# Kernel optimization log

Hardware: AMD Instinct MI355X
Metric: run time of the kernel (lower is better)

The kernel has to match this reference:

```python
import jax, jax.numpy as jnp
import numpy as np

B, T, D = 256, 512, 128   # batch, T_max, input_dim
Z, TR, EM, RH = 128, 256, 256, 512  # z_dim, trans_dim, emission_dim, rnn_dim


def _dkf_infer(x, y, eps_comb, eps_emit, rnn_Wih, rnn_Whh, rnn_bih, rnn_bhh, h0, zq0,
               tr_g1_W, tr_g1_b, tr_g2_W, tr_g2_b, tr_p1_W, tr_p1_b, tr_p2_W, tr_p2_b,
               tr_mu_W, tr_mu_b, tr_lv_W, tr_lv_b,
               cb_h_W, cb_h_b, cb_mu_W, cb_mu_b, cb_lv_W, cb_lv_b,
               em_h1_W, em_h1_b, em_h2_W, em_h2_b, em_mu_W, em_mu_b, em_logvar):
    b = x.shape[0]
    # --- nn.RNN (relu nonlinearity, batch_first), scanned time-major ---
    xw = jnp.einsum('btd,dh->tbh', x, rnn_Wih) + rnn_bih  # [T,B,RH] input projection hoisted out of scan

    def rnn_step(h, xw_t):
        h = jax.nn.relu(xw_t + h @ rnn_Whh + rnn_bhh)
        return h, h

    _, rnn_out = jax.lax.scan(rnn_step, jnp.broadcast_to(h0, (b, h0.shape[0])), xw)  # [T,B,RH]

    y_tm = jnp.swapaxes(y, 0, 1)  # [T,B,D]

    def step(z_prev, inp):
        h_rnn, yt, e_cb, e_em = inp
        # GatedTransition (infer only uses prior mu/logvar; its sample is discarded)
        gate = jax.nn.sigmoid(jax.nn.relu(z_prev @ tr_g1_W + tr_g1_b) @ tr_g2_W + tr_g2_b)
        prop = jax.nn.relu(z_prev @ tr_p1_W + tr_p1_b) @ tr_p2_W + tr_p2_b
        pr_mu = (1.0 - gate) * (z_prev @ tr_mu_W + tr_mu_b) + gate * prop
        pr_lv = jax.nn.relu(prop) @ tr_lv_W + tr_lv_b
        # Combiner + reparameterization
        hc = 0.5 * (jnp.tanh(z_prev @ cb_h_W + cb_h_b) + h_rnn)
        mu = hc @ cb_mu_W + cb_mu_b
        lv = hc @ cb_lv_W + cb_lv_b
        z_t = mu + e_cb * jnp.exp(0.5 * lv)
        # Emitter + reparameterization
        h1 = jax.nn.relu(z_t @ em_h1_W + em_h1_b)
        h2 = jax.nn.relu(h1 @ em_h2_W + em_h2_b)
        x_mu = h2 @ em_mu_W + em_mu_b
        x_t = x_mu + e_em * jnp.exp(0.5 * em_logvar)
        # KL(q || prior) summed over z, per batch element
        kl = jnp.sum(0.5 * (pr_lv - lv + (jnp.exp(lv) + (mu - pr_mu) ** 2) / jnp.exp(pr_lv) - 1.0), axis=1)
        # per-element MSE reduced over x_dim
        rec = jnp.mean((x_t - yt) ** 2, axis=1)
        return z_t, (kl, rec)

    z0 = jnp.broadcast_to(zq0, (b, zq0.shape[0]))
    _, (kl_states, rec_losses) = jax.lax.scan(step, z0, (rnn_out, y_tm, eps_comb, eps_emit))
    return jnp.stack([jnp.mean(rec_losses), jnp.mean(kl_states)])  # [rec_loss, kl_loss]


def setup_inputs() -> dict:
    key = jax.random.key(0)
    ks = iter(jax.random.split(key, 32))
    nrm = lambda shape, s=0.05: jax.random.normal(next(ks), shape, dtype=jnp.float32) * s
    z = lambda *shape: jnp.zeros(shape, jnp.float32)
    return dict(
        x=nrm((B, T, D), 1.0), y=nrm((B, T, D), 1.0),
        eps_comb=nrm((T, B, Z), 1.0), eps_emit=nrm((T, B, D), 1.0),
        rnn_Wih=nrm((D, RH)), rnn_Whh=nrm((RH, RH)), rnn_bih=z(RH), rnn_bhh=z(RH),
        h0=z(RH), zq0=z(Z),
        tr_g1_W=nrm((Z, TR)), tr_g1_b=z(TR), tr_g2_W=nrm((TR, Z)), tr_g2_b=z(Z),
        tr_p1_W=nrm((Z, TR)), tr_p1_b=z(TR), tr_p2_W=nrm((TR, Z)), tr_p2_b=z(Z),
        tr_mu_W=jnp.eye(Z, dtype=jnp.float32), tr_mu_b=z(Z),  # identity init as in torch code
        tr_lv_W=nrm((Z, Z)), tr_lv_b=z(Z),
        cb_h_W=nrm((Z, RH)), cb_h_b=z(RH),
        cb_mu_W=nrm((RH, Z)), cb_mu_b=z(Z),
        cb_lv_W=nrm((RH, Z)), cb_lv_b=z(Z),
        em_h1_W=nrm((Z, EM)), em_h1_b=z(EM),
        em_h2_W=nrm((EM, EM)), em_h2_b=z(EM),
        em_mu_W=nrm((EM, D)), em_mu_b=z(D),
        em_logvar=jnp.ones((D,), jnp.float32),  # nn.Parameter(torch.ones(input_dim))
    )


def reference(x, y, eps_comb, eps_emit, rnn_Wih, rnn_Whh, rnn_bih, rnn_bhh, h0, zq0,
              tr_g1_W, tr_g1_b, tr_g2_W, tr_g2_b, tr_p1_W, tr_p1_b, tr_p2_W, tr_p2_b,
              tr_mu_W, tr_mu_b, tr_lv_W, tr_lv_b,
              cb_h_W, cb_h_b, cb_mu_W, cb_mu_b, cb_lv_W, cb_lv_b,
              em_h1_W, em_h1_b, em_h2_W, em_h2_b, em_mu_W, em_mu_b, em_logvar):
    return _dkf_infer(x, y, eps_comb, eps_emit, rnn_Wih, rnn_Whh, rnn_bih, rnn_bhh, h0, zq0,
                      tr_g1_W, tr_g1_b, tr_g2_W, tr_g2_b, tr_p1_W, tr_p1_b, tr_p2_W, tr_p2_b,
                      tr_mu_W, tr_mu_b, tr_lv_W, tr_lv_b,
                      cb_h_W, cb_h_b, cb_mu_W, cb_mu_b, cb_lv_W, cb_lv_b,
                      em_h1_W, em_h1_b, em_h2_W, em_h2_b, em_mu_W, em_mu_b, em_logvar)
```

## Files before the change

kernel.cpp:

```cpp
#include <hip/hip_runtime.h>


#define T_LEN 512
#define BATCH 256
#define DIMX  128
#define ZDIM  128
#define RHD   512
#define CHUNK 32

typedef _Float16 f16;
typedef _Float16 f16x4 __attribute__((ext_vector_type(4)));
typedef _Float16 f16x8 __attribute__((ext_vector_type(8)));
typedef float    f32x4 __attribute__((ext_vector_type(4)));

#define MFMA16(a,b,c) __builtin_amdgcn_mfma_f32_16x16x32_f16((a),(b),(c),0,0,0)

#define PK_WIH  0u
#define PK_WHH  65536u
#define PK_G1   327680u
#define PK_G2   360448u
#define PK_P1   393216u
#define PK_P2   425984u
#define PK_TMU  458752u
#define PK_TLV  475136u
#define PK_CBH  491520u
#define PK_CBML 557056u
#define PK_E1   688128u
#define PK_E2   720896u
#define PK_EMU  786432u

#define WS_XW   0ull
#define WS_Z    (WS_XW  + 134217728ull)
#define WS_MU   (WS_Z   + 33619968ull)
#define WS_LV   (WS_MU  + 33554432ull)
#define WS_PK   (WS_LV  + 33554432ull)
#define WS_PART (WS_PK  + 1638400ull)
#define WS_PROG (WS_PART + 16384ull)
#define WS_END  (WS_PROG + 256ull)

__device__ __forceinline__ void ldsfence() {
  asm volatile("s_waitcnt lgkmcnt(0)" ::: "memory");
  __builtin_amdgcn_sched_barrier(0);
}

__device__ __forceinline__ void lbar() {
  asm volatile("s_waitcnt lgkmcnt(0)" ::: "memory");
  __builtin_amdgcn_s_barrier();
  asm volatile("" ::: "memory");
}

__device__ __forceinline__ void pin8(f16x8& v) {
  f32x4 t = __builtin_bit_cast(f32x4, v);
  asm volatile("" : "+v"(t));
  v = __builtin_bit_cast(f16x8, t);
}

template<int N>
__device__ __forceinline__ void zacc(f32x4* a) {
  f32x4 z = {0.f, 0.f, 0.f, 0.f};
#pragma unroll
  for (int i = 0; i < N; ++i) a[i] = z;
}

__device__ __forceinline__ f16x8 cvt8(const float* p) {
  float4 a = *(const float4*)p, b = *(const float4*)(p + 4);
  f16x8 r;
  r[0] = (f16)a.x; r[1] = (f16)a.y; r[2] = (f16)a.z; r[3] = (f16)a.w;
  r[4] = (f16)b.x; r[5] = (f16)b.y; r[6] = (f16)b.z; r[7] = (f16)b.w;
  return r;
}

__device__ __forceinline__ int swz(int row, int col) {
  return (row << 9) + (col ^ ((row & 7) << 3));
}
__device__ __forceinline__ int swz128(int row, int col) {
  return (row << 7) + (col ^ ((row & 7) << 3));
}

template<int KS>
__device__ __forceinline__ void load_af(const f16* src, int sstr, int lane, f16x8* af) {
#pragma unroll
  for (int ks = 0; ks < KS; ++ks)
    af[ks] = *(const f16x8*)(src + (lane & 15) * sstr + ks * 32 + ((lane >> 4) << 3));
}

template<int KS, int NT>
__device__ __forceinline__ void gemm_regA(const f16x8* af, const f16* __restrict__ bp,
                                          int lane, f32x4* acc) {
#pragma unroll
  for (int ks = 0; ks < KS; ++ks)
#pragma unroll
    for (int j = 0; j < NT; ++j) {
      f16x8 bf = *(const f16x8*)(bp + (((size_t)(ks * NT + j)) << 9) + (lane << 3));
      acc[j] = MFMA16(af[ks], bf, acc[j]);
    }
}

template<int NT>
__device__ __forceinline__ void store_relu(const f32x4* acc, const float* __restrict__ bias,
                                           f16* dst, int dstr, int lane) {
  int colv = lane & 15, rb = (lane >> 4) << 2;
#pragma unroll
  for (int j = 0; j < NT; ++j)
#pragma unroll
    for (int r = 0; r < 4; ++r)
      dst[(rb + r) * dstr + j * 16 + colv] = (f16)fmaxf(acc[j][r] + bias[j * 16 + colv], 0.f);
}

struct PackEnt { const float* s1; const float* s2; int nsplit, K, N; unsigned dst, wg0; };
struct PackTab { PackEnt e[13]; };

__global__ void pack_all_kernel(PackTab tb, f16* __restrict__ pk) {
  int i = 0;
#pragma unroll
  for (int k = 1; k < 13; ++k)
    if (blockIdx.x >= tb.e[k].wg0) i = k;
  const PackEnt& E = tb.e[i];
  int idx = (blockIdx.x - E.wg0) * 256 + threadIdx.x;
  if (idx >= E.K * E.N) return;
  int j = idx & 7, l = (idx >> 3) & 63, fi = idx >> 9;
  int NTt = E.N >> 4;
  int nt = fi % NTt, ks = fi / NTt;
  int k = ks * 32 + ((l >> 4) << 3) + j;
  int n = (nt << 4) + (l & 15);
  float v;
  if (n < E.nsplit) v = E.s1[(size_t)k * E.nsplit + n];
  else              v = E.s2[(size_t)k * (E.N - E.nsplit) + (n - E.nsplit)];
  pk[E.dst + idx] = (f16)v;
}

__global__ void zero_prog_kernel(unsigned* __restrict__ p) {
  if (threadIdx.x < 16)
    __hip_atomic_store(p + threadIdx.x, 0u, __ATOMIC_RELAXED, __HIP_MEMORY_SCOPE_AGENT);
}

__global__ __launch_bounds__(256) void xw_kernel(
    const float* __restrict__ x, const f16* __restrict__ pk,
    const float* __restrict__ bih, const float* __restrict__ bhh,
    f16* __restrict__ xw) {
  __shared__ float bs[512];
  const int tid = threadIdx.x, lane = tid & 63, w = tid >> 6;
  const int colv = lane & 15, l4 = lane >> 4;
  const int m0 = blockIdx.x * 64 + w * 16;
  const int t = m0 >> 8, b0 = m0 & 255;
  for (int i = tid; i < 512; i += 256) bs[i] = bih[i] + bhh[i];
  __syncthreads();
  f16x8 xB[4];
  const float* xr = x + ((size_t)(b0 + colv) * T_LEN + t) * DIMX;
#pragma unroll
  for (int ks = 0; ks < 4; ++ks) xB[ks] = cvt8(xr + ks * 32 + l4 * 8);
  f32x4 acc[32]; zacc<32>(acc);
#pragma unroll
  for (int ks = 0; ks < 4; ++ks)
#pragma unroll
    for (int mt = 0; mt < 32; ++mt)
      acc[mt] = MFMA16(*(const f16x8*)(pk + PK_WIH + ((size_t)(ks * 32 + mt) << 9) + (lane << 3)),
                       xB[ks], acc[mt]);
  f16* xo = xw + ((size_t)t * BATCH + b0 + colv) * RHD;
#pragma unroll
  for (int mt = 0; mt < 32; ++mt) {
    f16x4 v;
#pragma unroll
    for (int r = 0; r < 4; ++r) v[r] = (f16)(acc[mt][r] + bs[mt * 16 + l4 * 4 + r]);
    *(f16x4*)(xo + mt * 16 + l4 * 4) = v;
  }
}

__global__ __launch_bounds__(256, 1) void scan_pipe_kernel(
    const f16* __restrict__ pk, const float* __restrict__ h0,
    const float* __restrict__ zq0, const float* __restrict__ chb,
    const float* __restrict__ cmb, const float* __restrict__ clb,
    const float* __restrict__ eps_comb, f16* __restrict__ xw,
    f16* __restrict__ z_all, f16* __restrict__ mu_all, f16* __restrict__ lv_all,
    unsigned* __restrict__ prog) {
  __shared__ __align__(16) f16 lds[73728];
  const int tid = threadIdx.x, lane = tid & 63, w = tid >> 6;
  const int colv = lane & 15, l4 = lane >> 4;

  if (blockIdx.x < 16) {
    const int g = blockIdx.x, b0 = g * 16;
    f16* whh_lds = lds;
    f16* h_st = lds + 65536;
    {
      const uint4* src = (const uint4*)(pk + PK_WHH + 196608u);
      for (int i = tid; i < 8192; i += 256) ((uint4*)whh_lds)[i] = src[i];
    }
    f16x8 whhA[8][12];
#pragma unroll
    for (int mt = 0; mt < 8; ++mt)
#pragma unroll
      for (int ks = 0; ks < 12; ++ks) {
        whhA[mt][ks] = *(const f16x8*)(pk + PK_WHH +
            ((size_t)(ks * 32 + w * 8 + mt) << 9) + (lane << 3));
        pin8(whhA[mt][ks]);
      }
    for (int i = tid; i < 8192; i += 256) h_st[swz(i >> 9, i & 511)] = (f16)h0[i & 511];
    __syncthreads();

    const int moff = w * 128 + l4 * 4;
    f16* xp = xw + (size_t)(b0 + colv) * RHD;
    f16x4 xwc[8], xwn[8];
#pragma unroll
    for (int mt = 0; mt < 8; ++mt) xwc[mt] = *(const f16x4*)(xp + moff + mt * 16);

    for (int c = 0; c < T_LEN / CHUNK; ++c) {
#pragma unroll 1
      for (int tt = 0; tt < CHUNK; ++tt) {
        int t = c * CHUNK + tt;
        f16* xpn = (t < T_LEN - 1) ? xp + (size_t)BATCH * RHD : xp;
#pragma unroll
        for (int mt = 0; mt < 8; ++mt) xwn[mt] = *(const f16x4*)(xpn + moff + mt * 16);
        f32x4 acc[8]; zacc<8>(acc);
#pragma unroll
        for (int ks = 0; ks < 12; ++ks) {
          f16x8 B = *(const f16x8*)&h_st[swz(colv, ks * 32 + l4 * 8)];
#pragma unroll
          for (int mt = 0; mt < 8; ++mt) acc[mt] = MFMA16(whhA[mt][ks], B, acc[mt]);
        }
#pragma unroll
        for (int ks = 0; ks < 4; ++ks) {
          f16x8 B = *(const f16x8*)&h_st[swz(colv, (12 + ks) * 32 + l4 * 8)];
#pragma unroll
          for (int mt = 0; mt < 8; ++mt)
            acc[mt] = MFMA16(*(const f16x8*)(whh_lds +
                (((ks * 32 + w * 8 + mt) << 6) + lane) * 8), B, acc[mt]);
        }
        lbar();
#pragma unroll
        for (int mt = 0; mt < 8; ++mt) {
          f16x4 h4;
#pragma unroll
          for (int r = 0; r < 4; ++r)
            h4[r] = (f16)fmaxf(acc[mt][r] + (float)xwc[mt][r], 0.f);
          *(f16x4*)&h_st[swz(colv, moff + mt * 16)] = h4;
          *(f16x4*)(xp + moff + mt * 16) = h4;
        }
        lbar();
        xp = xpn;
#pragma unroll
        for (int mt = 0; mt < 8; ++mt) xwc[mt] = xwn[mt];
      }
      __syncthreads();
      if (tid == 0)
        __hip_atomic_store(prog + g, (unsigned)(c + 1), __ATOMIC_RELEASE,
                           __HIP_MEMORY_SCOPE_AGENT);
    }
  } else {
    const int g = blockIdx.x - 16, b0 = g * 16;
    f16* cbml_lds = lds;
    f16* hc_st = lds + 32768;
    f16* z_st  = lds + 40960;
    f16* m_st  = lds + 43008;
    {
      const uint4* src = (const uint4*)(pk + PK_CBML + 98304u);
      for (int i = tid; i < 4096; i += 256) ((uint4*)cbml_lds)[i] = src[i];
    }
    f16x8 cbhA[8][4];
#pragma unroll
    for (int mt = 0; mt < 8; ++mt)
#pragma unroll
      for (int ks = 0; ks < 4; ++ks) {
        cbhA[mt][ks] = *(const f16x8*)(pk + PK_CBH +
            ((size_t)(ks * 32 + w * 8 + mt) << 9) + (lane << 3));
        pin8(cbhA[mt][ks]);
      }
    f16x8 cbmlA[4][12];
#pragma unroll
    for (int mt = 0; mt < 4; ++mt)
#pragma unroll
      for (int ks = 0; ks < 12; ++ks) {
        cbmlA[mt][ks] = *(const f16x8*)(pk + PK_CBML +
            ((size_t)(ks * 16 + w * 4 + mt) << 9) + (lane << 3));
        pin8(cbmlA[mt][ks]);
      }
    f16x4 chbv[8];
#pragma unroll
    for (int mt = 0; mt < 8; ++mt)
#pragma unroll
      for (int r = 0; r < 4; ++r)
        chbv[mt][r] = (f16)chb[(w * 8 + mt) * 16 + l4 * 4 + r];
    float mb[4][4];
#pragma unroll
    for (int mt = 0; mt < 4; ++mt)
#pragma unroll
      for (int r = 0; r < 4; ++r) {
        int d = (w * 4 + mt) * 16 + l4 * 4 + r;
        mb[mt][r] = (d < 128) ? cmb[d] : clb[d - 128];
      }
    for (int i = tid; i < 2048; i += 256) {
      f16 zv = (f16)zq0[i & 127];
      z_st[swz128(i >> 7, i & 127)] = zv;
      z_all[(size_t)(b0 + (i >> 7)) * ZDIM + (i & 127)] = zv;
    }
    __syncthreads();

    const int moff = w * 128 + l4 * 4;
    const int m2off = w * 64 + l4 * 4;
    const int be = tid >> 4, d0 = (tid & 15) * 8;
    const f16* hp = xw + (size_t)(b0 + colv) * RHD;
    const float* epb = eps_comb + (size_t)(b0 + be) * ZDIM + d0;
    f16x4 hv[8];
    float4 ep0, ep1, epn0, epn1;

    for (int c = 0; c < T_LEN / CHUNK; ++c) {
      if (tid == 0) {
        while (__hip_atomic_load(prog + g, __ATOMIC_RELAXED,
                                 __HIP_MEMORY_SCOPE_AGENT) < (unsigned)(c + 1))
          __builtin_amdgcn_s_sleep(2);
      }
      __syncthreads();
      __builtin_amdgcn_fence(__ATOMIC_ACQUIRE, "agent");
      {
        const f16* hpt = hp + (size_t)(c * CHUNK) * BATCH * RHD;
#pragma unroll
        for (int mt = 0; mt < 8; ++mt) hv[mt] = *(const f16x4*)(hpt + moff + mt * 16);
        const float* ept = epb + (size_t)(c * CHUNK) * BATCH * ZDIM;
        ep0 = *(const float4*)ept; ep1 = *(const float4*)(ept + 4);
      }
#pragma unroll 1
      for (int tt = 0; tt < CHUNK; ++tt) {
        int t = c * CHUNK + tt;
        f16x8 zB[4];
#pragma unroll
        for (int ks = 0; ks < 4; ++ks)
          zB[ks] = *(const f16x8*)&z_st[swz128(colv, ks * 32 + l4 * 8)];
        f32x4 a1[8]; zacc<8>(a1);
#pragma unroll
        for (int ks = 0; ks < 4; ++ks)
#pragma unroll
          for (int mt = 0; mt < 8; ++mt) a1[mt] = MFMA16(cbhA[mt][ks], zB[ks], a1[mt]);
#pragma unroll
        for (int mt = 0; mt < 8; ++mt) {
          f16x4 hc4;
#pragma unroll
          for (int r = 0; r < 4; ++r) {
            float cs = a1[mt][r] + (float)chbv[mt][r];
            float ex = __builtin_amdgcn_exp2f(cs * 2.885390082f);
            float th = 1.f - 2.f * __builtin_amdgcn_rcpf(ex + 1.f);
            hc4[r] = (f16)(0.5f * (th + (float)hv[mt][r]));
          }
          *(f16x4*)&hc_st[swz(colv, moff + mt * 16)] = hc4;
        }
        lbar();
        if (tt < CHUNK - 1) {
          const f16* hpt = hp + (size_t)(t + 1) * BATCH * RHD;
#pragma unroll
          for (int mt = 0; mt < 8; ++mt) hv[mt] = *(const f16x4*)(hpt + moff + mt * 16);
          const float* ept = epb + (size_t)(t + 1) * BATCH * ZDIM;
          epn0 = *(const float4*)ept; epn1 = *(const float4*)(ept + 4);
        }
        f32x4 a2[4]; zacc<4>(a2);
#pragma unroll
        for (int ks = 0; ks < 12; ++ks) {
          f16x8 hcB = *(const f16x8*)&hc_st[swz(colv, ks * 32 + l4 * 8)];
#pragma unroll
          for (int mt = 0; mt < 4; ++mt) a2[mt] = MFMA16(cbmlA[mt][ks], hcB, a2[mt]);
        }
#pragma unroll
        for (int ks = 0; ks < 4; ++ks) {
          f16x8 hcB = *(const f16x8*)&hc_st[swz(colv, (12 + ks) * 32 + l4 * 8)];
#pragma unroll
          for (int mt = 0; mt < 4; ++mt)
            a2[mt] = MFMA16(*(const f16x8*)(cbml_lds +
                (((ks * 16 + w * 4 + mt) << 6) + lane) * 8), hcB, a2[mt]);
        }
#pragma unroll
        for (int mt = 0; mt < 4; ++mt) {
          f16x4 v;
#pragma unroll
          for (int r = 0; r < 4; ++r) v[r] = (f16)(a2[mt][r] + mb[mt][r]);
          *(f16x4*)&m_st[colv * 264 + m2off + mt * 16] = v;
        }
        lbar();
        {
          f16x8 mu8 = *(const f16x8*)&m_st[be * 264 + d0];
          f16x8 lv8 = *(const f16x8*)&m_st[be * 264 + 128 + d0];
          float epv[8] = {ep0.x, ep0.y, ep0.z, ep0.w, ep1.x, ep1.y, ep1.z, ep1.w};
          f16x8 z8;
#pragma unroll
          for (int r = 0; r < 8; ++r) {
            float mu = (float)mu8[r], lv = (float)lv8[r];
            z8[r] = (f16)(mu + epv[r] * __builtin_amdgcn_exp2f(lv * 0.7213475204f));
          }
          *(f16x8*)&z_st[swz128(be, d0)] = z8;
          size_t o = ((size_t)t * BATCH + b0 + be) * ZDIM + d0;
          *(f16x8*)(z_all + o + (size_t)BATCH * ZDIM) = z8;
          *(f16x8*)(mu_all + o) = mu8;
          *(f16x8*)(lv_all + o) = lv8;
        }
        lbar();
        ep0 = epn0; ep1 = epn1;
      }
    }
  }
}

__global__ __launch_bounds__(256) void dpar_kernel(
    const f16* __restrict__ z_all, const f16* __restrict__ mu_all,
    const f16* __restrict__ lv_all, const float* __restrict__ y,
    const float* __restrict__ eps_emit, const f16* __restrict__ pk,
    const float* __restrict__ g1b, const float* __restrict__ g2b,
    const float* __restrict__ p1b, const float* __restrict__ p2b,
    const float* __restrict__ tmub, const float* __restrict__ tlvb,
    const float* __restrict__ e1b, const float* __restrict__ e2b,
    const float* __restrict__ emub, const float* __restrict__ em_logvar,
    float* __restrict__ partials) {
  __shared__ __align__(16) f16 sb256[4][16 * 264];
  __shared__ __align__(16) f16 sb128[4][16 * 136];
  __shared__ float wsum[4][2];
  const int tid = threadIdx.x, lane = tid & 63, w = tid >> 6;
  const int colv = lane & 15, rb = (lane >> 4) << 2;
  const int m0 = blockIdx.x * 64 + w * 16;
  const int t = m0 >> 8, b0 = m0 & 255;
  f16* B256 = &sb256[w][0];
  f16* B128 = &sb128[w][0];

  f16x8 zp[4], zt[4];
  const f16* zpr = z_all + ((size_t)t * BATCH + b0) * ZDIM;
#pragma unroll
  for (int ks = 0; ks < 4; ++ks) {
    zp[ks] = *(const f16x8*)(zpr + (size_t)colv * ZDIM + ks * 32 + ((lane >> 4) << 3));
    zt[ks] = *(const f16x8*)(zpr + (size_t)BATCH * ZDIM + (size_t)colv * ZDIM + ks * 32 + ((lane >> 4) << 3));
  }

  f32x4 a16[16], a8[8];
  f16x8 af[8], af4[4];
  zacc<16>(a16); gemm_regA<4, 16>(zp, pk + PK_G1, lane, a16);
  store_relu<16>(a16, g1b, B256, 264, lane); ldsfence();
  load_af<8>(B256, 264, lane, af); ldsfence();
  zacc<8>(a8); gemm_regA<8, 8>(af, pk + PK_G2, lane, a8);
  f32x4 gate[8];
#pragma unroll
  for (int j = 0; j < 8; ++j)
#pragma unroll
    for (int r = 0; r < 4; ++r)
      gate[j][r] = 1.f / (1.f + expf(-(a8[j][r] + g2b[j * 16 + colv])));
  zacc<16>(a16); gemm_regA<4, 16>(zp, pk + PK_P1, lane, a16);
  store_relu<16>(a16, p1b, B256, 264, lane); ldsfence();
  load_af<8>(B256, 264, lane, af); ldsfence();
  zacc<8>(a8); gemm_regA<8, 8>(af, pk + PK_P2, lane, a8);
  f32x4 prop[8];
#pragma unroll
  for (int j = 0; j < 8; ++j)
#pragma unroll
    for (int r = 0; r < 4; ++r) {
      float v = a8[j][r] + p2b[j * 16 + colv];
      prop[j][r] = v;
      B128[(rb + r) * 136 + j * 16 + colv] = (f16)fmaxf(v, 0.f);
    }
  ldsfence();
  zacc<8>(a8); gemm_regA<4, 8>(zp, pk + PK_TMU, lane, a8);
  f32x4 prmu[8];
#pragma unroll
  for (int j = 0; j < 8; ++j)
#pragma unroll
    for (int r = 0; r < 4; ++r) {
      float gg = gate[j][r];
      prmu[j][r] = (1.f - gg) * (a8[j][r] + tmub[j * 16 + colv]) + gg * prop[j][r];
    }
  load_af<4>(B128, 136, lane, af4); ldsfence();
  zacc<8>(a8); gemm_regA<4, 8>(af4, pk + PK_TLV, lane, a8);
  f32x4 prlv[8];
#pragma unroll
  for (int j = 0; j < 8; ++j)
#pragma unroll
    for (int r = 0; r < 4; ++r) prlv[j][r] = a8[j][r] + tlvb[j * 16 + colv];
  zacc<16>(a16); gemm_regA<4, 16>(zt, pk + PK_E1, lane, a16);
  store_relu<16>(a16, e1b, B256, 264, lane); ldsfence();
  load_af<8>(B256, 264, lane, af); ldsfence();
  zacc<16>(a16); gemm_regA<8, 16>(af, pk + PK_E2, lane, a16);
  store_relu<16>(a16, e2b, B256, 264, lane); ldsfence();
  load_af<8>(B256, 264, lane, af); ldsfence();
  zacc<8>(a8); gemm_regA<8, 8>(af, pk + PK_EMU, lane, a8);
  float srec = 0.f, skl = 0.f;
#pragma unroll
  for (int j = 0; j < 8; ++j)
#pragma unroll
    for (int r = 0; r < 4; ++r) {
      int row = rb + r, n = j * 16 + colv;
      size_t tb = (size_t)t * BATCH + b0 + row;
      float xt = a8[j][r] + emub[n] + eps_emit[tb * DIMX + n] * expf(0.5f * em_logvar[n]);
      float dy = xt - y[((size_t)(b0 + row) * T_LEN + t) * DIMX + n];
      srec += dy * dy;
      float m_ = (float)mu_all[tb * ZDIM + n], l_ = (float)lv_all[tb * ZDIM + n];
      float dm = m_ - prmu[j][r];
      skl += 0.5f * (prlv[j][r] - l_ + (expf(l_) + dm * dm) * expf(-prlv[j][r]) - 1.f);
    }
#pragma unroll
  for (int off = 32; off; off >>= 1) {
    srec += __shfl_xor(srec, off);
    skl += __shfl_xor(skl, off);
  }
  if (lane == 0) { wsum[w][0] = srec; wsum[w][1] = skl; }
  __syncthreads();
  if (tid == 0) {
    partials[blockIdx.x * 2 + 0] = wsum[0][0] + wsum[1][0] + wsum[2][0] + wsum[3][0];
    partials[blockIdx.x * 2 + 1] = wsum[0][1] + wsum[1][1] + wsum[2][1] + wsum[3][1];
  }
}

__global__ void finalize_kernel(const float* __restrict__ partials, float* __restrict__ out) {
  __shared__ float sm[256][2];
  int tid = threadIdx.x;
  float r = 0.f, kk = 0.f;
  for (int i = tid; i < 2048; i += 256) {
    r += partials[2 * i];
    kk += partials[2 * i + 1];
  }
  sm[tid][0] = r; sm[tid][1] = kk;
  __syncthreads();
  for (int off = 128; off; off >>= 1) {
    if (tid < off) { sm[tid][0] += sm[tid + off][0]; sm[tid][1] += sm[tid + off][1]; }
    __syncthreads();
  }
  if (tid == 0) {
    out[0] = sm[0][0] / (131072.f * 128.f);
    out[1] = sm[0][1] / 131072.f;
  }
}

extern "C" void kernel_launch(void* const* d_in, const int* in_sizes, int n_in,
                              void* d_out, int out_size, void* d_ws, size_t ws_size,
                              hipStream_t stream) {
  (void)in_sizes; (void)n_in; (void)out_size;
  const float* x        = (const float*)d_in[0];
  const float* y        = (const float*)d_in[1];
  const float* eps_comb = (const float*)d_in[2];
  const float* eps_emit = (const float*)d_in[3];
  const float* wih = (const float*)d_in[4];
  const float* whh = (const float*)d_in[5];
  const float* bih = (const float*)d_in[6];
  const float* bhh = (const float*)d_in[7];
  const float* h0  = (const float*)d_in[8];
  const float* zq0 = (const float*)d_in[9];
  const float* g1W = (const float*)d_in[10]; const float* g1b = (const float*)d_in[11];
  const float* g2W = (const float*)d_in[12]; const float* g2b = (const float*)d_in[13];
  const float* p1W = (const float*)d_in[14]; const float* p1b = (const float*)d_in[15];
  const float* p2W = (const float*)d_in[16]; const float* p2b = (const float*)d_in[17];
  const float* tmuW = (const float*)d_in[18]; const float* tmub = (const float*)d_in[19];
  const float* tlvW = (const float*)d_in[20]; const float* tlvb = (const float*)d_in[21];
  const float* chW = (const float*)d_in[22]; const float* chb = (const float*)d_in[23];
  const float* cmW = (const float*)d_in[24]; const float* cmb = (const float*)d_in[25];
  const float* clW = (const float*)d_in[26]; const float* clb = (const float*)d_in[27];
  const float* e1W = (const float*)d_in[28]; const float* e1b = (const float*)d_in[29];
  const float* e2W = (const float*)d_in[30]; const float* e2b = (const float*)d_in[31];
  const float* emW = (const float*)d_in[32]; const float* emb = (const float*)d_in[33];
  const float* elv = (const float*)d_in[34];

  char* ws = (char*)d_ws;
  f16*  xw      = (f16*)(ws + WS_XW);
  f16*  z_all   = (f16*)(ws + WS_Z);
  f16*  mu_all  = (f16*)(ws + WS_MU);
  f16*  lv_all  = (f16*)(ws + WS_LV);
  f16*  pk      = (f16*)(ws + WS_PK);
  float* partials = (float*)(ws + WS_PART);
  unsigned* prog  = (unsigned*)(ws + WS_PROG);
  float* out = (float*)d_out;
  if (ws_size < WS_END) return;

  zero_prog_kernel<<<dim3(1), dim3(32), 0, stream>>>(prog);

  PackTab tb;
  unsigned wg = 0; int ei = 0;
#define PACK(S1, S2, NS_, K_, N_, OFF) \
  tb.e[ei] = PackEnt{S1, S2, NS_, K_, N_, OFF, wg}; wg += (unsigned)((K_) * (N_)) / 256; ++ei;
  PACK(wih, wih, 512, 128, 512, PK_WIH);
  PACK(whh, whh, 512, 512, 512, PK_WHH);
  PACK(g1W, g1W, 256, 128, 256, PK_G1);
  PACK(g2W, g2W, 128, 256, 128, PK_G2);
  PACK(p1W, p1W, 256, 128, 256, PK_P1);
  PACK(p2W, p2W, 128, 256, 128, PK_P2);
  PACK(tmuW, tmuW, 128, 128, 128, PK_TMU);
  PACK(tlvW, tlvW, 128, 128, 128, PK_TLV);
  PACK(chW, chW, 512, 128, 512, PK_CBH);
  PACK(cmW, clW, 128, 512, 256, PK_CBML);
  PACK(e1W, e1W, 256, 128, 256, PK_E1);
  PACK(e2W, e2W, 256, 256, 256, PK_E2);
  PACK(emW, emW, 128, 256, 128, PK_EMU);
#undef PACK
  pack_all_kernel<<<dim3(wg), dim3(256), 0, stream>>>(tb, pk);

  xw_kernel<<<dim3(2048), dim3(256), 0, stream>>>(x, pk, bih, bhh, xw);
  scan_pipe_kernel<<<dim3(32), dim3(256), 0, stream>>>(
      pk, h0, zq0, chb, cmb, clb, eps_comb, xw, z_all, mu_all, lv_all, prog);
  dpar_kernel<<<dim3(2048), dim3(256), 0, stream>>>(z_all, mu_all, lv_all, y, eps_emit, pk,
                                                    g1b, g2b, p1b, p2b, tmub, tlvb, e1b, e2b,
                                                    emb, elv, partials);
  finalize_kernel<<<dim3(1), dim3(256), 0, stream>>>(partials, out);
}
```

Measured before the change: 2.523 ms.

## Fuse input projection, recurrent scan and loss kernel into one persistent pipelined kernel

```diff
diff --git a/kernel.cpp b/kernel.cpp
--- a/kernel.cpp
+++ b/kernel.cpp
@@ -7,6 +7,7 @@
 #define ZDIM  128
 #define RHD   512
 #define CHUNK 32
+#define NWKR  224
 
 typedef _Float16 f16;
 typedef _Float16 f16x4 __attribute__((ext_vector_type(4)));
@@ -105,6 +106,10 @@
 #pragma unroll
     for (int r = 0; r < 4; ++r)
       dst[(rb + r) * dstr + j * 16 + colv] = (f16)fmaxf(acc[j][r] + bias[j * 16 + colv], 0.f);
+}
+
+__device__ __forceinline__ unsigned ldflag(const unsigned* p) {
+  return __hip_atomic_load(p, __ATOMIC_RELAXED, __HIP_MEMORY_SCOPE_AGENT);
 }
 
 struct PackEnt { const float* s1; const float* s2; int nsplit, K, N; unsigned dst, wg0; };
@@ -130,52 +135,31 @@
 }
 
 __global__ void zero_prog_kernel(unsigned* __restrict__ p) {
-  if (threadIdx.x < 16)
+  if (threadIdx.x < 48)
     __hip_atomic_store(p + threadIdx.x, 0u, __ATOMIC_RELAXED, __HIP_MEMORY_SCOPE_AGENT);
 }
 
-__global__ __launch_bounds__(256) void xw_kernel(
-    const float* __restrict__ x, const f16* __restrict__ pk,
-    const float* __restrict__ bih, const float* __restrict__ bhh,
-    f16* __restrict__ xw) {
-  __shared__ float bs[512];
-  const int tid = threadIdx.x, lane = tid & 63, w = tid >> 6;
-  const int colv = lane & 15, l4 = lane >> 4;
-  const int m0 = blockIdx.x * 64 + w * 16;
-  const int t = m0 >> 8, b0 = m0 & 255;
-  for (int i = tid; i < 512; i += 256) bs[i] = bih[i] + bhh[i];
-  __syncthreads();
-  f16x8 xB[4];
-  const float* xr = x + ((size_t)(b0 + colv) * T_LEN + t) * DIMX;
-#pragma unroll
-  for (int ks = 0; ks < 4; ++ks) xB[ks] = cvt8(xr + ks * 32 + l4 * 8);
-  f32x4 acc[32]; zacc<32>(acc);
-#pragma unroll
-  for (int ks = 0; ks < 4; ++ks)
-#pragma unroll
-    for (int mt = 0; mt < 32; ++mt)
-      acc[mt] = MFMA16(*(const f16x8*)(pk + PK_WIH + ((size_t)(ks * 32 + mt) << 9) + (lane << 3)),
-                       xB[ks], acc[mt]);
-  f16* xo = xw + ((size_t)t * BATCH + b0 + colv) * RHD;
-#pragma unroll
-  for (int mt = 0; mt < 32; ++mt) {
-    f16x4 v;
-#pragma unroll
-    for (int r = 0; r < 4; ++r) v[r] = (f16)(acc[mt][r] + bs[mt * 16 + l4 * 4 + r]);
-    *(f16x4*)(xo + mt * 16 + l4 * 4) = v;
-  }
-}
-
-__global__ __launch_bounds__(256, 1) void scan_pipe_kernel(
+__global__ __launch_bounds__(256, 1) void fused_kernel(
     const f16* __restrict__ pk, const float* __restrict__ h0,
     const float* __restrict__ zq0, const float* __restrict__ chb,
     const float* __restrict__ cmb, const float* __restrict__ clb,
     const float* __restrict__ eps_comb, f16* __restrict__ xw,
     f16* __restrict__ z_all, f16* __restrict__ mu_all, f16* __restrict__ lv_all,
-    unsigned* __restrict__ prog) {
+    const float* __restrict__ x, const float* __restrict__ bih,
+    const float* __restrict__ bhh, const float* __restrict__ y,
+    const float* __restrict__ eps_emit,
+    const float* __restrict__ g1b, const float* __restrict__ g2b,
+    const float* __restrict__ p1b, const float* __restrict__ p2b,
+    const float* __restrict__ tmub, const float* __restrict__ tlvb,
+    const float* __restrict__ e1b, const float* __restrict__ e2b,
+    const float* __restrict__ emub, const float* __restrict__ em_logvar,
+    float* __restrict__ partials, unsigned* __restrict__ flags) {
   __shared__ __align__(16) f16 lds[73728];
   const int tid = threadIdx.x, lane = tid & 63, w = tid >> 6;
   const int colv = lane & 15, l4 = lane >> 4;
+  unsigned* prog  = flags;
+  unsigned* zprog = flags + 16;
+  unsigned* xcnt  = flags + 32;
 
   if (blockIdx.x < 16) {
     const int g = blockIdx.x, b0 = g * 16;
@@ -197,6 +181,10 @@
     for (int i = tid; i < 8192; i += 256) h_st[swz(i >> 9, i & 511)] = (f16)h0[i & 511];
     __syncthreads();
 
+    if (tid == 0) { while (ldflag(xcnt + 0) < 128u) __builtin_amdgcn_s_sleep(2); }
+    __syncthreads();
+    __builtin_amdgcn_fence(__ATOMIC_ACQUIRE, "agent");
+
     const int moff = w * 128 + l4 * 4;
     f16* xp = xw + (size_t)(b0 + colv) * RHD;
     f16x4 xwc[8], xwn[8];
@@ -204,6 +192,10 @@
     for (int mt = 0; mt < 8; ++mt) xwc[mt] = *(const f16x4*)(xp + moff + mt * 16);
 
     for (int c = 0; c < T_LEN / CHUNK; ++c) {
+      const int cw = (c + 1 < 16) ? c + 1 : 15;
+      if (tid == 0) { while (ldflag(xcnt + cw) < 128u) __builtin_amdgcn_s_sleep(2); }
+      __syncthreads();
+      __builtin_amdgcn_fence(__ATOMIC_ACQUIRE, "agent");
 #pragma unroll 1
       for (int tt = 0; tt < CHUNK; ++tt) {
         int t = c * CHUNK + tt;
@@ -245,7 +237,7 @@
         __hip_atomic_store(prog + g, (unsigned)(c + 1), __ATOMIC_RELEASE,
                            __HIP_MEMORY_SCOPE_AGENT);
     }
-  } else {
+  } else if (blockIdx.x < 32) {
     const int g = blockIdx.x - 16, b0 = g * 16;
     f16* cbml_lds = lds;
     f16* hc_st = lds + 32768;
@@ -304,9 +296,7 @@
 
     for (int c = 0; c < T_LEN / CHUNK; ++c) {
       if (tid == 0) {
-        while (__hip_atomic_load(prog + g, __ATOMIC_RELAXED,
-                                 __HIP_MEMORY_SCOPE_AGENT) < (unsigned)(c + 1))
-          __builtin_amdgcn_s_sleep(2);
+        while (ldflag(prog + g) < (unsigned)(c + 1)) __builtin_amdgcn_s_sleep(2);
       }
       __syncthreads();
       __builtin_amdgcn_fence(__ATOMIC_ACQUIRE, "agent");
@@ -391,111 +381,149 @@
         lbar();
         ep0 = epn0; ep1 = epn1;
       }
-    }
-  }
-}
-
-__global__ __launch_bounds__(256) void dpar_kernel(
-    const f16* __restrict__ z_all, const f16* __restrict__ mu_all,
-    const f16* __restrict__ lv_all, const float* __restrict__ y,
-    const float* __restrict__ eps_emit, const f16* __restrict__ pk,
-    const float* __restrict__ g1b, const float* __restrict__ g2b,
-    const float* __restrict__ p1b, const float* __restrict__ p2b,
-    const float* __restrict__ tmub, const float* __restrict__ tlvb,
-    const float* __restrict__ e1b, const float* __restrict__ e2b,
-    const float* __restrict__ emub, const float* __restrict__ em_logvar,
-    float* __restrict__ partials) {
-  __shared__ __align__(16) f16 sb256[4][16 * 264];
-  __shared__ __align__(16) f16 sb128[4][16 * 136];
-  __shared__ float wsum[4][2];
-  const int tid = threadIdx.x, lane = tid & 63, w = tid >> 6;
-  const int colv = lane & 15, rb = (lane >> 4) << 2;
-  const int m0 = blockIdx.x * 64 + w * 16;
-  const int t = m0 >> 8, b0 = m0 & 255;
-  f16* B256 = &sb256[w][0];
-  f16* B128 = &sb128[w][0];
-
-  f16x8 zp[4], zt[4];
-  const f16* zpr = z_all + ((size_t)t * BATCH + b0) * ZDIM;
-#pragma unroll
-  for (int ks = 0; ks < 4; ++ks) {
-    zp[ks] = *(const f16x8*)(zpr + (size_t)colv * ZDIM + ks * 32 + ((lane >> 4) << 3));
-    zt[ks] = *(const f16x8*)(zpr + (size_t)BATCH * ZDIM + (size_t)colv * ZDIM + ks * 32 + ((lane >> 4) << 3));
-  }
-
-  f32x4 a16[16], a8[8];
-  f16x8 af[8], af4[4];
-  zacc<16>(a16); gemm_regA<4, 16>(zp, pk + PK_G1, lane, a16);
-  store_relu<16>(a16, g1b, B256, 264, lane); ldsfence();
-  load_af<8>(B256, 264, lane, af); ldsfence();
-  zacc<8>(a8); gemm_regA<8, 8>(af, pk + PK_G2, lane, a8);
-  f32x4 gate[8];
-#pragma unroll
-  for (int j = 0; j < 8; ++j)
-#pragma unroll
-    for (int r = 0; r < 4; ++r)
-      gate[j][r] = 1.f / (1.f + expf(-(a8[j][r] + g2b[j * 16 + colv])));
-  zacc<16>(a16); gemm_regA<4, 16>(zp, pk + PK_P1, lane, a16);
-  store_relu<16>(a16, p1b, B256, 264, lane); ldsfence();
-  load_af<8>(B256, 264, lane, af); ldsfence();
-  zacc<8>(a8); gemm_regA<8, 8>(af, pk + PK_P2, lane, a8);
-  f32x4 prop[8];
-#pragma unroll
-  for (int j = 0; j < 8; ++j)
-#pragma unroll
-    for (int r = 0; r < 4; ++r) {
-      float v = a8[j][r] + p2b[j * 16 + colv];
-      prop[j][r] = v;
-      B128[(rb + r) * 136 + j * 16 + colv] = (f16)fmaxf(v, 0.f);
-    }
-  ldsfence();
-  zacc<8>(a8); gemm_regA<4, 8>(zp, pk + PK_TMU, lane, a8);
-  f32x4 prmu[8];
-#pragma unroll
-  for (int j = 0; j < 8; ++j)
-#pragma unroll
-    for (int r = 0; r < 4; ++r) {
-      float gg = gate[j][r];
-      prmu[j][r] = (1.f - gg) * (a8[j][r] + tmub[j * 16 + colv]) + gg * prop[j][r];
-    }
-  load_af<4>(B128, 136, lane, af4); ldsfence();
-  zacc<8>(a8); gemm_regA<4, 8>(af4, pk + PK_TLV, lane, a8);
-  f32x4 prlv[8];
-#pragma unroll
-  for (int j = 0; j < 8; ++j)
-#pragma unroll
-    for (int r = 0; r < 4; ++r) prlv[j][r] = a8[j][r] + tlvb[j * 16 + colv];
-  zacc<16>(a16); gemm_regA<4, 16>(zt, pk + PK_E1, lane, a16);
-  store_relu<16>(a16, e1b, B256, 264, lane); ldsfence();
-  load_af<8>(B256, 264, lane, af); ldsfence();
-  zacc<16>(a16); gemm_regA<8, 16>(af, pk + PK_E2, lane, a16);
-  store_relu<16>(a16, e2b, B256, 264, lane); ldsfence();
-  load_af<8>(B256, 264, lane, af); ldsfence();
-  zacc<8>(a8); gemm_regA<8, 8>(af, pk + PK_EMU, lane, a8);
-  float srec = 0.f, skl = 0.f;
-#pragma unroll
-  for (int j = 0; j < 8; ++j)
-#pragma unroll
-    for (int r = 0; r < 4; ++r) {
-      int row = rb + r, n = j * 16 + colv;
-      size_t tb = (size_t)t * BATCH + b0 + row;
-      float xt = a8[j][r] + emub[n] + eps_emit[tb * DIMX + n] * expf(0.5f * em_logvar[n]);
-      float dy = xt - y[((size_t)(b0 + row) * T_LEN + t) * DIMX + n];
-      srec += dy * dy;
-      float m_ = (float)mu_all[tb * ZDIM + n], l_ = (float)lv_all[tb * ZDIM + n];
-      float dm = m_ - prmu[j][r];
-      skl += 0.5f * (prlv[j][r] - l_ + (expf(l_) + dm * dm) * expf(-prlv[j][r]) - 1.f);
-    }
-#pragma unroll
-  for (int off = 32; off; off >>= 1) {
-    srec += __shfl_xor(srec, off);
-    skl += __shfl_xor(skl, off);
-  }
-  if (lane == 0) { wsum[w][0] = srec; wsum[w][1] = skl; }
-  __syncthreads();
-  if (tid == 0) {
-    partials[blockIdx.x * 2 + 0] = wsum[0][0] + wsum[1][0] + wsum[2][0] + wsum[3][0];
-    partials[blockIdx.x * 2 + 1] = wsum[0][1] + wsum[1][1] + wsum[2][1] + wsum[3][1];
+      __syncthreads();
+      if (tid == 0)
+        __hip_atomic_store(zprog + g, (unsigned)(c + 1), __ATOMIC_RELEASE,
+                           __HIP_MEMORY_SCOPE_AGENT);
+    }
+  } else {
+    const int wkr = blockIdx.x - 32;
+    float* bs = (float*)lds;
+    for (int i = tid; i < 512; i += 256) bs[i] = bih[i] + bhh[i];
+    __syncthreads();
+    for (int i = wkr; i < 2048; i += NWKR) {
+      const int m0 = i * 64 + w * 16;
+      const int t = m0 >> 8, b0 = m0 & 255;
+      f16x8 xB[4];
+      const float* xr = x + ((size_t)(b0 + colv) * T_LEN + t) * DIMX;
+#pragma unroll
+      for (int ks = 0; ks < 4; ++ks) xB[ks] = cvt8(xr + ks * 32 + l4 * 8);
+      f32x4 acc[32]; zacc<32>(acc);
+#pragma unroll
+      for (int ks = 0; ks < 4; ++ks)
+#pragma unroll
+        for (int mt = 0; mt < 32; ++mt)
+          acc[mt] = MFMA16(*(const f16x8*)(pk + PK_WIH +
+              ((size_t)(ks * 32 + mt) << 9) + (lane << 3)), xB[ks], acc[mt]);
+      f16* xo = xw + ((size_t)t * BATCH + b0 + colv) * RHD;
+#pragma unroll
+      for (int mt = 0; mt < 32; ++mt) {
+        f16x4 v;
+#pragma unroll
+        for (int r = 0; r < 4; ++r) v[r] = (f16)(acc[mt][r] + bs[mt * 16 + l4 * 4 + r]);
+        *(f16x4*)(xo + mt * 16 + l4 * 4) = v;
+      }
+      __syncthreads();
+      if (tid == 0)
+        __hip_atomic_fetch_add(xcnt + (i >> 7), 1u, __ATOMIC_RELEASE,
+                               __HIP_MEMORY_SCOPE_AGENT);
+    }
+    for (int j = wkr; j < 2048; j += NWKR) {
+      const int m0 = j * 64 + w * 16;
+      const int t = m0 >> 8, b0 = m0 & 255;
+      const int c = j >> 7;
+      const int gb = (j & 3) * 4;
+      if (tid == 0) {
+        const unsigned need = (unsigned)(c + 1);
+        for (;;) {
+          unsigned a = ldflag(zprog + gb), b = ldflag(zprog + gb + 1);
+          unsigned cc = ldflag(zprog + gb + 2), d = ldflag(zprog + gb + 3);
+          unsigned mn = min(min(a, b), min(cc, d));
+          if (mn >= need) break;
+          __builtin_amdgcn_s_sleep(32);
+        }
+      }
+      __syncthreads();
+      __builtin_amdgcn_fence(__ATOMIC_ACQUIRE, "agent");
+
+      f16* B256 = lds + w * 4224;
+      f16* B128 = lds + 16896 + w * 2176;
+      float* wsum = (float*)(lds + 25600);
+      const int rb = (lane >> 4) << 2;
+
+      f16x8 zp[4], zt[4];
+      const f16* zpr = z_all + ((size_t)t * BATCH + b0) * ZDIM;
+#pragma unroll
+      for (int ks = 0; ks < 4; ++ks) {
+        zp[ks] = *(const f16x8*)(zpr + (size_t)colv * ZDIM + ks * 32 + (l4 << 3));
+        zt[ks] = *(const f16x8*)(zpr + (size_t)BATCH * ZDIM + (size_t)colv * ZDIM + ks * 32 + (l4 << 3));
+      }
+      f32x4 a16[16], a8[8];
+      f16x8 af[8], af4[4];
+      zacc<16>(a16); gemm_regA<4, 16>(zp, pk + PK_G1, lane, a16);
+      store_relu<16>(a16, g1b, B256, 264, lane); ldsfence();
+      load_af<8>(B256, 264, lane, af); ldsfence();
+      zacc<8>(a8); gemm_regA<8, 8>(af, pk + PK_G2, lane, a8);
+      f32x4 gate[8];
+#pragma unroll
+      for (int jj = 0; jj < 8; ++jj)
+#pragma unroll
+        for (int r = 0; r < 4; ++r)
+          gate[jj][r] = 1.f / (1.f + expf(-(a8[jj][r] + g2b[jj * 16 + colv])));
+      zacc<16>(a16); gemm_regA<4, 16>(zp, pk + PK_P1, lane, a16);
+      store_relu<16>(a16, p1b, B256, 264, lane); ldsfence();
+      load_af<8>(B256, 264, lane, af); ldsfence();
+      zacc<8>(a8); gemm_regA<8, 8>(af, pk + PK_P2, lane, a8);
+      f32x4 prop[8];
+#pragma unroll
+      for (int jj = 0; jj < 8; ++jj)
+#pragma unroll
+        for (int r = 0; r < 4; ++r) {
+          float v = a8[jj][r] + p2b[jj * 16 + colv];
+          prop[jj][r] = v;
+          B128[(rb + r) * 136 + jj * 16 + colv] = (f16)fmaxf(v, 0.f);
+        }
+      ldsfence();
+      zacc<8>(a8); gemm_regA<4, 8>(zp, pk + PK_TMU, lane, a8);
+      f32x4 prmu[8];
+#pragma unroll
+      for (int jj = 0; jj < 8; ++jj)
+#pragma unroll
+        for (int r = 0; r < 4; ++r) {
+          float gg = gate[jj][r];
+          prmu[jj][r] = (1.f - gg) * (a8[jj][r] + tmub[jj * 16 + colv]) + gg * prop[jj][r];
+        }
+      load_af<4>(B128, 136, lane, af4); ldsfence();
+      zacc<8>(a8); gemm_regA<4, 8>(af4, pk + PK_TLV, lane, a8);
+      f32x4 prlv[8];
+#pragma unroll
+      for (int jj = 0; jj < 8; ++jj)
+#pragma unroll
+        for (int r = 0; r < 4; ++r) prlv[jj][r] = a8[jj][r] + tlvb[jj * 16 + colv];
+      zacc<16>(a16); gemm_regA<4, 16>(zt, pk + PK_E1, lane, a16);
+      store_relu<16>(a16, e1b, B256, 264, lane); ldsfence();
+      load_af<8>(B256, 264, lane, af); ldsfence();
+      zacc<16>(a16); gemm_regA<8, 16>(af, pk + PK_E2, lane, a16);
+      store_relu<16>(a16, e2b, B256, 264, lane); ldsfence();
+      load_af<8>(B256, 264, lane, af); ldsfence();
+      zacc<8>(a8); gemm_regA<8, 8>(af, pk + PK_EMU, lane, a8);
+      float srec = 0.f, skl = 0.f;
+#pragma unroll
+      for (int jj = 0; jj < 8; ++jj)
+#pragma unroll
+        for (int r = 0; r < 4; ++r) {
+          int row = rb + r, n = jj * 16 + colv;
+          size_t tb = (size_t)t * BATCH + b0 + row;
+          float xt = a8[jj][r] + emub[n] + eps_emit[tb * DIMX + n] * expf(0.5f * em_logvar[n]);
+          float dy = xt - y[((size_t)(b0 + row) * T_LEN + t) * DIMX + n];
+          srec += dy * dy;
+          float m_ = (float)mu_all[tb * ZDIM + n], l_ = (float)lv_all[tb * ZDIM + n];
+          float dm = m_ - prmu[jj][r];
+          skl += 0.5f * (prlv[jj][r] - l_ + (expf(l_) + dm * dm) * expf(-prlv[jj][r]) - 1.f);
+        }
+#pragma unroll
+      for (int off = 32; off; off >>= 1) {
+        srec += __shfl_xor(srec, off);
+        skl += __shfl_xor(skl, off);
+      }
+      if (lane == 0) { wsum[w * 2] = srec; wsum[w * 2 + 1] = skl; }
+      __syncthreads();
+      if (tid == 0) {
+        partials[j * 2 + 0] = wsum[0] + wsum[2] + wsum[4] + wsum[6];
+        partials[j * 2 + 1] = wsum[1] + wsum[3] + wsum[5] + wsum[7];
+      }
+      __syncthreads();
+    }
   }
 }
 
@@ -554,11 +582,11 @@
   f16*  lv_all  = (f16*)(ws + WS_LV);
   f16*  pk      = (f16*)(ws + WS_PK);
   float* partials = (float*)(ws + WS_PART);
-  unsigned* prog  = (unsigned*)(ws + WS_PROG);
+  unsigned* flags = (unsigned*)(ws + WS_PROG);
   float* out = (float*)d_out;
   if (ws_size < WS_END) return;
 
-  zero_prog_kernel<<<dim3(1), dim3(32), 0, stream>>>(prog);
+  zero_prog_kernel<<<dim3(1), dim3(64), 0, stream>>>(flags);
 
   PackTab tb;
   unsigned wg = 0; int ei = 0;
@@ -580,11 +608,10 @@
 #undef PACK
   pack_all_kernel<<<dim3(wg), dim3(256), 0, stream>>>(tb, pk);
 
-  xw_kernel<<<dim3(2048), dim3(256), 0, stream>>>(x, pk, bih, bhh, xw);
-  scan_pipe_kernel<<<dim3(32), dim3(256), 0, stream>>>(
-      pk, h0, zq0, chb, cmb, clb, eps_comb, xw, z_all, mu_all, lv_all, prog);
-  dpar_kernel<<<dim3(2048), dim3(256), 0, stream>>>(z_all, mu_all, lv_all, y, eps_emit, pk,
-                                                    g1b, g2b, p1b, p2b, tmub, tlvb, e1b, e2b,
-                                                    emb, elv, partials);
+  fused_kernel<<<dim3(256), dim3(256), 0, stream>>>(
+      pk, h0, zq0, chb, cmb, clb, eps_comb, xw, z_all, mu_all, lv_all,
+      x, bih, bhh, y, eps_emit,
+      g1b, g2b, p1b, p2b, tmub, tlvb, e1b, e2b, emb, elv,
+      partials, flags);
   finalize_kernel<<<dim3(1), dim3(256), 0, stream>>>(partials, out);
 }
```

Result: slower. 3.095 ms (+22.7%).

## Remap combiner mu/logvar tiles per wave to drop LDS staging round-trip

Applied to the files above, without the earlier changes.

```diff
diff --git a/kernel.cpp b/kernel.cpp
--- a/kernel.cpp
+++ b/kernel.cpp
@@ -105,6 +105,10 @@
 #pragma unroll
     for (int r = 0; r < 4; ++r)
       dst[(rb + r) * dstr + j * 16 + colv] = (f16)fmaxf(acc[j][r] + bias[j * 16 + colv], 0.f);
+}
+
+__device__ __forceinline__ unsigned ldflag(const unsigned* p) {
+  return __hip_atomic_load(p, __ATOMIC_RELAXED, __HIP_MEMORY_SCOPE_AGENT);
 }
 
 struct PackEnt { const float* s1; const float* s2; int nsplit, K, N; unsigned dst, wg0; };
@@ -130,7 +134,7 @@
 }
 
 __global__ void zero_prog_kernel(unsigned* __restrict__ p) {
-  if (threadIdx.x < 16)
+  if (threadIdx.x < 64)
     __hip_atomic_store(p + threadIdx.x, 0u, __ATOMIC_RELAXED, __HIP_MEMORY_SCOPE_AGENT);
 }
 
@@ -250,7 +254,6 @@
     f16* cbml_lds = lds;
     f16* hc_st = lds + 32768;
     f16* z_st  = lds + 40960;
-    f16* m_st  = lds + 43008;
     {
       const uint4* src = (const uint4*)(pk + PK_CBML + 98304u);
       for (int i = tid; i < 4096; i += 256) ((uint4*)cbml_lds)[i] = src[i];
@@ -264,14 +267,16 @@
             ((size_t)(ks * 32 + w * 8 + mt) << 9) + (lane << 3));
         pin8(cbhA[mt][ks]);
       }
+    int ntj[4];
+    ntj[0] = 2 * w; ntj[1] = 2 * w + 1; ntj[2] = 8 + 2 * w; ntj[3] = 9 + 2 * w;
     f16x8 cbmlA[4][12];
 #pragma unroll
-    for (int mt = 0; mt < 4; ++mt)
+    for (int j = 0; j < 4; ++j)
 #pragma unroll
       for (int ks = 0; ks < 12; ++ks) {
-        cbmlA[mt][ks] = *(const f16x8*)(pk + PK_CBML +
-            ((size_t)(ks * 16 + w * 4 + mt) << 9) + (lane << 3));
-        pin8(cbmlA[mt][ks]);
+        cbmlA[j][ks] = *(const f16x8*)(pk + PK_CBML +
+            ((size_t)(ks * 16 + ntj[j]) << 9) + (lane << 3));
+        pin8(cbmlA[j][ks]);
       }
     f16x4 chbv[8];
 #pragma unroll
@@ -279,13 +284,14 @@
 #pragma unroll
       for (int r = 0; r < 4; ++r)
         chbv[mt][r] = (f16)chb[(w * 8 + mt) * 16 + l4 * 4 + r];
-    float mb[4][4];
-#pragma unroll
-    for (int mt = 0; mt < 4; ++mt)
+    float mbm[2][4], mbl[2][4];
+#pragma unroll
+    for (int j = 0; j < 2; ++j)
 #pragma unroll
       for (int r = 0; r < 4; ++r) {
-        int d = (w * 4 + mt) * 16 + l4 * 4 + r;
-        mb[mt][r] = (d < 128) ? cmb[d] : clb[d - 128];
+        int d = (2 * w + j) * 16 + l4 * 4 + r;
+        mbm[j][r] = cmb[d];
+        mbl[j][r] = clb[d];
       }
     for (int i = tid; i < 2048; i += 256) {
       f16 zv = (f16)zq0[i & 127];
@@ -295,18 +301,14 @@
     __syncthreads();
 
     const int moff = w * 128 + l4 * 4;
-    const int m2off = w * 64 + l4 * 4;
-    const int be = tid >> 4, d0 = (tid & 15) * 8;
     const f16* hp = xw + (size_t)(b0 + colv) * RHD;
-    const float* epb = eps_comb + (size_t)(b0 + be) * ZDIM + d0;
+    const float* epbase = eps_comb + (size_t)(b0 + colv) * ZDIM;
     f16x4 hv[8];
-    float4 ep0, ep1, epn0, epn1;
+    float4 epc[2], epn[2];
 
     for (int c = 0; c < T_LEN / CHUNK; ++c) {
       if (tid == 0) {
-        while (__hip_atomic_load(prog + g, __ATOMIC_RELAXED,
-                                 __HIP_MEMORY_SCOPE_AGENT) < (unsigned)(c + 1))
-          __builtin_amdgcn_s_sleep(2);
+        while (ldflag(prog + g) < (unsigned)(c + 1)) __builtin_amdgcn_s_sleep(2);
       }
       __syncthreads();
       __builtin_amdgcn_fence(__ATOMIC_ACQUIRE, "agent");
@@ -314,8 +316,10 @@
         const f16* hpt = hp + (size_t)(c * CHUNK) * BATCH * RHD;
 #pragma unroll
         for (int mt = 0; mt < 8; ++mt) hv[mt] = *(const f16x4*)(hpt + moff + mt * 16);
-        const float* ept = epb + (size_t)(c * CHUNK) * BATCH * ZDIM;
-        ep0 = *(const float4*)ept; ep1 = *(const float4*)(ept + 4);
+        const float* ept = epbase + (size_t)(c * CHUNK) * BATCH * ZDIM;
+#pragma unroll
+        for (int j = 0; j < 2; ++j)
+          epc[j] = *(const float4*)(ept + (2 * w + j) * 16 + l4 * 4);
       }
 #pragma unroll 1
       for (int tt = 0; tt < CHUNK; ++tt) {
@@ -346,50 +350,46 @@
           const f16* hpt = hp + (size_t)(t + 1) * BATCH * RHD;
 #pragma unroll
           for (int mt = 0; mt < 8; ++mt) hv[mt] = *(const f16x4*)(hpt + moff + mt * 16);
-          const float* ept = epb + (size_t)(t + 1) * BATCH * ZDIM;
-          epn0 = *(const float4*)ept; epn1 = *(const float4*)(ept + 4);
+          const float* ept = epbase + (size_t)(t + 1) * BATCH * ZDIM;
+#pragma unroll
+          for (int j = 0; j < 2; ++j)
+            epn[j] = *(const float4*)(ept + (2 * w + j) * 16 + l4 * 4);
         }
         f32x4 a2[4]; zacc<4>(a2);
 #pragma unroll
         for (int ks = 0; ks < 12; ++ks) {
           f16x8 hcB = *(const f16x8*)&hc_st[swz(colv, ks * 32 + l4 * 8)];
 #pragma unroll
-          for (int mt = 0; mt < 4; ++mt) a2[mt] = MFMA16(cbmlA[mt][ks], hcB, a2[mt]);
+          for (int j = 0; j < 4; ++j) a2[j] = MFMA16(cbmlA[j][ks], hcB, a2[j]);
         }
 #pragma unroll
         for (int ks = 0; ks < 4; ++ks) {
           f16x8 hcB = *(const f16x8*)&hc_st[swz(colv, (12 + ks) * 32 + l4 * 8)];
 #pragma unroll
-          for (int mt = 0; mt < 4; ++mt)
-            a2[mt] = MFMA16(*(const f16x8*)(cbml_lds +
-                (((ks * 16 + w * 4 + mt) << 6) + lane) * 8), hcB, a2[mt]);
-        }
-#pragma unroll
-        for (int mt = 0; mt < 4; ++mt) {
-          f16x4 v;
-#pragma unroll
-          for (int r = 0; r < 4; ++r) v[r] = (f16)(a2[mt][r] + mb[mt][r]);
-          *(f16x4*)&m_st[colv * 264 + m2off + mt * 16] = v;
+          for (int j = 0; j < 4; ++j)
+            a2[j] = MFMA16(*(const f16x8*)(cbml_lds +
+                (((ks * 16 + ntj[j]) << 6) + lane) * 8), hcB, a2[j]);
+        }
+#pragma unroll
+        for (int j = 0; j < 2; ++j) {
+          const int dj = (2 * w + j) * 16 + l4 * 4;
+          float epv[4] = {epc[j].x, epc[j].y, epc[j].z, epc[j].w};
+          f16x4 mu4, lv4, z4;
+#pragma unroll
+          for (int r = 0; r < 4; ++r) {
+            float mu = a2[j][r] + mbm[j][r];
+            float lv = a2[2 + j][r] + mbl[j][r];
+            mu4[r] = (f16)mu; lv4[r] = (f16)lv;
+            z4[r] = (f16)(mu + epv[r] * __builtin_amdgcn_exp2f(lv * 0.7213475204f));
+          }
+          *(f16x4*)&z_st[swz128(colv, dj)] = z4;
+          size_t o = ((size_t)t * BATCH + b0 + colv) * ZDIM + dj;
+          *(f16x4*)(z_all + o + (size_t)BATCH * ZDIM) = z4;
+          *(f16x4*)(mu_all + o) = mu4;
+          *(f16x4*)(lv_all + o) = lv4;
         }
         lbar();
-        {
-          f16x8 mu8 = *(const f16x8*)&m_st[be * 264 + d0];
-          f16x8 lv8 = *(const f16x8*)&m_st[be * 264 + 128 + d0];
-          float epv[8] = {ep0.x, ep0.y, ep0.z, ep0.w, ep1.x, ep1.y, ep1.z, ep1.w};
-          f16x8 z8;
-#pragma unroll
-          for (int r = 0; r < 8; ++r) {
-            float mu = (float)mu8[r], lv = (float)lv8[r];
-            z8[r] = (f16)(mu + epv[r] * __builtin_amdgcn_exp2f(lv * 0.7213475204f));
-          }
-          *(f16x8*)&z_st[swz128(be, d0)] = z8;
-          size_t o = ((size_t)t * BATCH + b0 + be) * ZDIM + d0;
-          *(f16x8*)(z_all + o + (size_t)BATCH * ZDIM) = z8;
-          *(f16x8*)(mu_all + o) = mu8;
-          *(f16x8*)(lv_all + o) = lv8;
-        }
-        lbar();
-        ep0 = epn0; ep1 = epn1;
+        epc[0] = epn[0]; epc[1] = epn[1];
       }
     }
   }
@@ -558,7 +558,7 @@
   float* out = (float*)d_out;
   if (ws_size < WS_END) return;
 
-  zero_prog_kernel<<<dim3(1), dim3(32), 0, stream>>>(prog);
+  zero_prog_kernel<<<dim3(1), dim3(64), 0, stream>>>(prog);
 
   PackTab tb;
   unsigned wg = 0; int ei = 0;
```

After: 2.813 ms. 11.5% more time.
